# Kernel tuning notes

Measured on AMD Instinct MI355X. Metric: run time of the kernel, lower is better.

## Reference

```python
import jax, jax.numpy as jnp
import numpy as np

NUM_CLASSES = 80
STRIDES = (8, 16, 32)
FEAT_HW = ((80, 80), (40, 40), (20, 20))
B = 32
MAX_GT = 60


def setup_inputs() -> dict:
    key = jax.random.key(0)
    ks = jax.random.split(key, 6)
    feats = {}
    for i, (s, (h, w)) in enumerate(zip(STRIDES, FEAT_HW)):
        feats[f"feat{s}"] = jax.random.normal(ks[i], (B, 5 + NUM_CLASSES, h, w), jnp.float32)
    u = jax.random.uniform(ks[3], (B, MAX_GT, 4), jnp.float32)
    # cx,cy in [0,640), w,h in [8,128): realistic pixel-space gt boxes for a 640x640 image
    gt_boxes = jnp.concatenate([u[..., :2] * 640.0, u[..., 2:] * 120.0 + 8.0], -1)
    gt_classes = jax.random.randint(ks[4], (B, MAX_GT), 0, NUM_CLASSES)
    num_gts = jax.random.randint(ks[5], (B,), 1, MAX_GT + 1)
    return dict(feat8=feats["feat8"], feat16=feats["feat16"], feat32=feats["feat32"],
                gt_boxes=gt_boxes, gt_classes=gt_classes, num_gts=num_gts)


def _decode(feat, stride):
    # torch get_output_and_grid: xy=(raw+grid)*stride, wh=exp(raw)*stride
    b, c, h, w = feat.shape
    yv, xv = jnp.meshgrid(jnp.arange(h), jnp.arange(w), indexing="ij")
    gx = xv.reshape(-1).astype(feat.dtype)  # [H*W]
    gy = yv.reshape(-1).astype(feat.dtype)
    out = feat.reshape(b, c, h * w).transpose(0, 2, 1)  # [B,A,C]
    xy = (out[..., :2] + jnp.stack([gx, gy], -1)[None]) * stride
    wh = jnp.exp(out[..., 2:4]) * stride
    return jnp.concatenate([xy, wh, out[..., 4:]], -1), gx, gy


def _pair_iou(a, b):
    # a: [G,4] xywh, b: [A,4] xywh -> [G,A] IoU (bboxes_iou, xyxy=False)
    tl = jnp.maximum(a[:, None, :2] - a[:, None, 2:] * 0.5, b[None, :, :2] - b[None, :, 2:] * 0.5)
    br = jnp.minimum(a[:, None, :2] + a[:, None, 2:] * 0.5, b[None, :, :2] + b[None, :, 2:] * 0.5)
    en = jnp.all(tl < br, -1)
    inter = jnp.where(en, jnp.prod(br - tl, -1), 0.0)
    area_a = jnp.prod(a[:, 2:], -1)
    area_b = jnp.prod(b[:, 2:], -1)
    return inter / (area_a[:, None] + area_b[None, :] - inter + 1e-16)


def _bce_logits(x, t):
    return jnp.maximum(x, 0.0) - x * t + jnp.log1p(jnp.exp(-jnp.abs(x)))


def _iou_loss(pred, tgt):
    # IOUloss(loss_type='iou'): 1 - iou^2, per box
    tl = jnp.maximum(pred[..., :2] - pred[..., 2:] * 0.5, tgt[..., :2] - tgt[..., 2:] * 0.5)
    br = jnp.minimum(pred[..., :2] + pred[..., 2:] * 0.5, tgt[..., :2] + tgt[..., 2:] * 0.5)
    en = jnp.all(tl < br, -1)
    inter = jnp.where(en, jnp.prod(br - tl, -1), 0.0)
    union = jnp.prod(pred[..., 2:], -1) + jnp.prod(tgt[..., 2:], -1) - inter
    iou = inter / (union + 1e-16)
    return 1.0 - iou ** 2


def _assign(boxes, cls_lo, obj_lo, gtb, gtc, vmask, cx, cy, st):
    # SimOTA per image. boxes [A,4], cls_lo [A,C], obj_lo [A], gtb [G,4], gtc [G] int,
    # vmask [G] bool (gt padding), cx/cy/st [A] anchor centers & strides.
    G, A = gtb.shape[0], boxes.shape[0]
    iou = _pair_iou(gtb, boxes)  # [G,A]
    gx, gy = gtb[:, :1], gtb[:, 1:2]
    gw, gh = gtb[:, 2:3], gtb[:, 3:4]
    in_box = ((cx[None] > gx - 0.5 * gw) & (cx[None] < gx + 0.5 * gw) &
              (cy[None] > gy - 0.5 * gh) & (cy[None] < gy + 0.5 * gh))
    R = 2.5  # center sampling radius (in strides)
    in_ctr = ((cx[None] > gx - R * st[None]) & (cx[None] < gx + R * st[None]) &
              (cy[None] > gy - R * st[None]) & (cy[None] < gy + R * st[None]))
    fg = ((in_box | in_ctr) & vmask[:, None]).any(0)  # [A] candidate anchors
    in_both = (in_box & in_ctr).astype(boxes.dtype)
    # pairwise cls cost: BCE(sqrt(sig(cls)*sig(obj)), onehot(gt_cls)).sum(-1),
    # decomposed to avoid the [G,A,C] tensor: sum_c bce0 + (bce1-bce0)[gt_cls]
    p = jnp.clip(jnp.sqrt(jax.nn.sigmoid(cls_lo) * jax.nn.sigmoid(obj_lo)[:, None]), 1e-7, 1.0 - 1e-7)
    bce1 = -jnp.log(p)          # [A,C]
    bce0 = -jnp.log(1.0 - p)    # [A,C]
    cls_cost = bce0.sum(-1)[None, :] + (bce1 - bce0)[:, gtc].T  # [G,A]
    cost = (cls_cost + 3.0 * (-jnp.log(iou + 1e-8))
            + 100000.0 * (1.0 - in_both)
            + 1e9 * (~fg)[None, :].astype(boxes.dtype)
            + 1e9 * (~vmask)[:, None].astype(boxes.dtype))
    K = 10  # n_candidate_k
    topk_ious, _ = jax.lax.top_k(iou * fg[None, :], K)
    dyn_k = jnp.maximum(topk_ious.sum(-1).astype(jnp.int32), 1)  # clamp(int(sum), min=1)
    _, pos = jax.lax.top_k(-cost, K)  # [G,K] lowest-cost anchors per gt
    sel = (jnp.arange(K)[None, :] < dyn_k[:, None]).astype(boxes.dtype)
    matching = jnp.zeros((G, A), boxes.dtype).at[jnp.arange(G)[:, None], pos].set(sel)
    matching = matching * vmask[:, None].astype(boxes.dtype)
    # resolve anchors claimed by >1 gt: keep min-cost gt
    conflict = matching.sum(0) > 1
    best_gt = jnp.argmin(cost, axis=0)  # [A]
    matching = jnp.where(conflict[None, :], jax.nn.one_hot(best_gt, G, dtype=matching.dtype).T, matching)
    fg_final = matching.sum(0) > 0  # [A]
    matched = jnp.argmax(matching, axis=0)  # [A]
    pred_iou = (matching * iou).sum(0)  # [A]
    cls_t = jax.nn.one_hot(gtc[matched], NUM_CLASSES, dtype=boxes.dtype) * pred_iou[:, None]
    reg_t = gtb[matched]
    return fg_final, cls_t, reg_t


def _forward(feat8, feat16, feat32, gt_boxes, gt_classes, num_gts):
    outs, cxs, cys, sts = [], [], [], []
    for f, s in zip((feat8, feat16, feat32), STRIDES):
        o, gx, gy = _decode(f, float(s))
        outs.append(o)
        cxs.append((gx + 0.5) * s)
        cys.append((gy + 0.5) * s)
        sts.append(jnp.full_like(gx, s))
    preds = jnp.concatenate(outs, 1)  # [B,A,5+C]
    cx = jnp.concatenate(cxs)
    cy = jnp.concatenate(cys)
    st = jnp.concatenate(sts)
    boxes = preds[..., :4]
    obj_lo = preds[..., 4]
    cls_lo = preds[..., 5:]
    vmask = jnp.arange(MAX_GT)[None, :] < num_gts[:, None]
    fg, cls_t, reg_t = jax.vmap(_assign, in_axes=(0, 0, 0, 0, 0, 0, None, None, None))(
        boxes, cls_lo, obj_lo, gt_boxes, gt_classes, vmask, cx, cy, st)
    # SimOTA assignment is no_grad in YOLOX: targets are constants wrt preds
    fg = jax.lax.stop_gradient(fg)
    cls_t = jax.lax.stop_gradient(cls_t)
    reg_t = jax.lax.stop_gradient(reg_t)
    fg_f = fg.astype(boxes.dtype)
    num_fg = jnp.maximum(fg_f.sum(), 1.0)
    loss_iou = (_iou_loss(boxes, reg_t) * fg_f).sum()
    loss_obj = _bce_logits(obj_lo, fg_f * 0.9).sum()  # obj_targets * 0.9 smoothing
    loss_cls = (_bce_logits(cls_lo, cls_t) * fg_f[..., None]).sum()
    REG_WEIGHT = 5.0
    return (REG_WEIGHT * loss_iou + loss_obj + loss_cls) / num_fg


def reference(feat8, feat16, feat32, gt_boxes, gt_classes, num_gts):
    return _forward(feat8, feat16, feat32, gt_boxes, gt_classes, num_gts)
```

## Files before the change

kernel.cpp:

```cpp
#include <hip/hip_runtime.h>

constexpr int kB = 32;
constexpr int kA = 8400;
constexpr int kG = 60;
constexpr int kC = 80;
constexpr int kK = 10;
constexpr int kNBx = (kA + 255)/256;
constexpr int kNB = kNBx * kB;

__device__ __forceinline__ float fexp(float x){ return __expf(x); }
__device__ __forceinline__ float flog(float x){ return __logf(x); }
__device__ __forceinline__ float frcp(float x){ return __builtin_amdgcn_rcpf(x); }
__device__ __forceinline__ float frsq(float x){ return __builtin_amdgcn_rsqf(x); }
__device__ __forceinline__ float fsqrt(float x){ return __builtin_amdgcn_sqrtf(x); }
__device__ __forceinline__ float fdiv(float a, float b){ return a * __builtin_amdgcn_rcpf(b); }
__device__ __forceinline__ float sigm(float x){ return frcp(1.0f + fexp(-x)); }
__device__ __forceinline__ float bce(float x, float t){
  return fmaxf(x, 0.0f) - x*t + flog(1.0f + fexp(-fabsf(x)));
}

__device__ __forceinline__ unsigned ordbits(float v){
  unsigned u = __float_as_uint(v);
  return (u & 0x80000000u) ? ~u : (u | 0x80000000u);
}
__device__ __forceinline__ float unpackf(unsigned k){
  return __uint_as_float((k & 0x80000000u) ? (k & 0x7fffffffu) : ~k);
}

struct AInfo { int x, y; float st; };
__device__ __forceinline__ AInfo ainfo(int a){
  AInfo r;
  if (a < 6400)      { r.x = a % 80;           r.y = a / 80;           r.st = 8.0f;  }
  else if (a < 8000) { int l = a-6400; r.x = l % 40; r.y = l / 40;     r.st = 16.0f; }
  else               { int l = a-8000; r.x = l % 20; r.y = l / 20;     r.st = 32.0f; }
  return r;
}

__device__ __forceinline__ float featv(const float* __restrict__ f8,
                                       const float* __restrict__ f16,
                                       const float* __restrict__ f32x,
                                       int b, int ch, int a){
  if (a < 6400) return f8 [(b*85 + ch)*6400 + a];
  if (a < 8000) return f16[(b*85 + ch)*1600 + (a - 6400)];
  return             f32x[(b*85 + ch)*400  + (a - 8000)];
}

__device__ __forceinline__ float pair_iou(float4 g, float4 p){
  float tlx = fmaxf(g.x - g.z*0.5f, p.x - p.z*0.5f);
  float tly = fmaxf(g.y - g.w*0.5f, p.y - p.w*0.5f);
  float brx = fminf(g.x + g.z*0.5f, p.x + p.z*0.5f);
  float bry = fminf(g.y + g.w*0.5f, p.y + p.w*0.5f);
  float inter = (tlx < brx && tly < bry) ? (brx-tlx)*(bry-tly) : 0.0f;
  return fdiv(inter, g.z*g.w + p.z*p.w - inter + 1e-16f);
}

__device__ __forceinline__ float cost_core(float iou, float cl, float obs, float b0sum,
                                           int a, float4 gt, int fg_a){
  AInfo ai = ainfo(a);
  float cx = ((float)ai.x + 0.5f)*ai.st;
  float cy = ((float)ai.y + 0.5f)*ai.st;
  bool in_box = (cx > gt.x - 0.5f*gt.z) && (cx < gt.x + 0.5f*gt.z)
             && (cy > gt.y - 0.5f*gt.w) && (cy < gt.y + 0.5f*gt.w);
  bool in_ctr = (cx > gt.x - 2.5f*ai.st) && (cx < gt.x + 2.5f*ai.st)
             && (cy > gt.y - 2.5f*ai.st) && (cy < gt.y + 2.5f*ai.st);
  float p = fsqrt(sigm(cl) * obs);
  p = fminf(fmaxf(p, 1e-7f), 1.0f - 1e-7f);
  float diff = -flog(p) + flog(1.0f - p);
  float c = b0sum + diff;
  c += 3.0f * (-flog(iou + 1e-8f));
  c += (in_box && in_ctr) ? 0.0f : 100000.0f;
  c += fg_a ? 0.0f : 1000000000.0f;
  return c;
}

__device__ __forceinline__ unsigned long long wave_max64(unsigned long long v){
  #pragma unroll
  for (int off = 32; off; off >>= 1){
    unsigned long long o = __shfl_xor(v, off, 64);
    if (o > v) v = o;
  }
  return v;
}

__device__ __forceinline__ void stage16(const float* g, float* l){
  __builtin_amdgcn_global_load_lds(
      (const __attribute__((address_space(1))) void*)g,
      (__attribute__((address_space(3))) void*)l, 16, 0, 0);
}
__device__ __forceinline__ void wait_vm6(int n){
  if      (n >= 6) asm volatile("s_waitcnt vmcnt(6)" ::: "memory");
  else if (n >= 4) asm volatile("s_waitcnt vmcnt(4)" ::: "memory");
  else if (n >= 2) asm volatile("s_waitcnt vmcnt(2)" ::: "memory");
  else             asm volatile("s_waitcnt vmcnt(0)" ::: "memory");
  __builtin_amdgcn_sched_barrier(0);
}
__device__ __forceinline__ void block_bar(){
  __builtin_amdgcn_sched_barrier(0);
  __builtin_amdgcn_s_barrier();
  __builtin_amdgcn_sched_barrier(0);
}

__global__ __launch_bounds__(256) void k_decode(
    const float* __restrict__ f8, const float* __restrict__ f16, const float* __restrict__ f32x,
    const float* __restrict__ gtb, const int* __restrict__ ngts,
    float* __restrict__ boxes, float* __restrict__ boxesZ,
    float* __restrict__ objl, float* __restrict__ b0s,
    float* __restrict__ bceS, float* __restrict__ obsA,
    int* __restrict__ fg, int* __restrict__ cnt, int* __restrict__ mtch){
  int b = blockIdx.y;
  int tid = threadIdx.x;
  int lane = tid & 63, wid = tid >> 6;
  int a0 = blockIdx.x*256 + tid;
  bool alive = (a0 < kA);
  int a = alive ? a0 : (kA - 1);
  __shared__ float4 sg[kG];
  __shared__ float buf[8][4][256];
  if (tid < kG) sg[tid] = ((const float4*)gtb)[b*kG + tid];
  int ng = ngts[b];
  __syncthreads();

  const float* base; int hw, off; float st_; int gx, gy;
  if (a < 6400)      { base=f8;   hw=6400; off=a;        st_=8.0f;  gx=off%80; gy=off/80; }
  else if (a < 8000) { base=f16;  hw=1600; off=a-6400;   st_=16.0f; gx=off%40; gy=off/40; }
  else               { base=f32x; hw=400;  off=a-8000;   st_=32.0f; gx=off%20; gy=off/20; }
  const float* p0 = base + ((size_t)b*85)*hw + off;

  float t0 = p0[0];
  float t1 = p0[(size_t)hw];
  float t2 = p0[(size_t)2*hw];
  float t3 = p0[(size_t)3*hw];
  float ob = p0[(size_t)4*hw];
  __builtin_amdgcn_sched_barrier(0);

  bool pure = (blockIdx.x < 31);
  const float* csrc = nullptr;
  size_t lhw = 0;
  if (pure){
    int ab = blockIdx.x*256;
    const float* lv; int lh, lo_;
    if (ab < 6400){ lv = f8;  lh = 6400; lo_ = ab; }
    else          { lv = f16; lh = 1600; lo_ = ab - 6400; }
    lhw = (size_t)lh;
    csrc = lv + ((size_t)b*85 + 5)*lh + lo_ + lane*4;
    #pragma unroll
    for (int u = 0; u < 8; ++u)
      stage16(csrc + (size_t)(4*u + wid)*lhw, &buf[u][wid][0]);
  }
  __builtin_amdgcn_sched_barrier(0);

  float4 bx;
  bx.x = (t0 + (float)gx) * st_;
  bx.y = (t1 + (float)gy) * st_;
  bx.z = fexp(t2) * st_;
  bx.w = fexp(t3) * st_;
  float obs = sigm(ob);
  float so = fsqrt(obs);
  float cx = ((float)gx + 0.5f)*st_;
  float cy = ((float)gy + 0.5f)*st_;
  int f = 0;
  for (int g = 0; g < ng; ++g){
    float4 gt = sg[g];
    bool in_box = (cx > gt.x - 0.5f*gt.z) && (cx < gt.x + 0.5f*gt.z)
               && (cy > gt.y - 0.5f*gt.w) && (cy < gt.y + 0.5f*gt.w);
    bool in_ctr = (cx > gt.x - 2.5f*st_) && (cx < gt.x + 2.5f*st_)
               && (cy > gt.y - 2.5f*st_) && (cy < gt.y + 2.5f*st_);
    if (in_box || in_ctr){ f = 1; break; }
  }

  float s = 0.0f, sumCl = 0.0f, slogv = 0.0f;
  if (pure){
    #pragma unroll
    for (int g = 0; g < 10; ++g){
      const int allowed = (g < 6) ? 6 : (18 - 2*g);
      wait_vm6(allowed);
      block_bar();
      float cv[8];
      #pragma unroll
      for (int c = 0; c < 4; ++c) cv[c]     = buf[(2*g)   & 7][c][tid];
      #pragma unroll
      for (int c = 0; c < 4; ++c) cv[4 + c] = buf[(2*g+1) & 7][c][tid];
      asm volatile("s_waitcnt lgkmcnt(0)" ::: "memory");
      __builtin_amdgcn_sched_barrier(0);
      block_bar();
      if (g < 6){
        stage16(csrc + (size_t)(4*(2*g+8) + wid)*lhw, &buf[(2*g)   & 7][wid][0]);
        stage16(csrc + (size_t)(4*(2*g+9) + wid)*lhw, &buf[(2*g+1) & 7][wid][0]);
      }
      __builtin_amdgcn_sched_barrier(0);
      float prodS = 1.0f, prodV = 1.0f;
      #pragma unroll
      for (int j = 0; j < 8; ++j){
        float c = cv[j];
        float u = fexp(-c);
        float v = 1.0f + u;
        float p = so * frsq(v);
        p = fminf(fmaxf(p, 1e-7f), 1.0f - 1e-7f);
        prodS *= (1.0f - p);
        prodV *= v;
        sumCl += c;
      }
      s -= flog(prodS);
      slogv += flog(prodV);
    }
  } else {
    const float* pc = p0 + (size_t)5*hw;
    #pragma unroll 1
    for (int grp = 0; grp < kC/8; ++grp){
      float prodS = 1.0f, prodV = 1.0f;
      #pragma unroll
      for (int j = 0; j < 8; ++j){
        float c = pc[(size_t)(grp*8 + j)*hw];
        float u = fexp(-c);
        float v = 1.0f + u;
        float p = so * frsq(v);
        p = fminf(fmaxf(p, 1e-7f), 1.0f - 1e-7f);
        prodS *= (1.0f - p);
        prodV *= v;
        sumCl += c;
      }
      s -= flog(prodS);
      slogv += flog(prodV);
    }
  }
  __builtin_amdgcn_sched_barrier(0);
  if (alive){
    int idx = b*kA + a;
    ((float4*)boxes)[idx] = bx;
    objl[idx] = ob;
    obsA[idx] = obs;
    cnt[idx] = 0;
    mtch[idx] = 0x7fffffff;
    fg[idx] = f;
    ((float4*)boxesZ)[idx] = f ? bx : make_float4(0.0f,0.0f,0.0f,0.0f);
    b0s[idx]  = s;
    bceS[idx] = sumCl + slogv;
  }
}

__global__ __launch_bounds__(256) void k_assign(
    const float* __restrict__ f8, const float* __restrict__ f16, const float* __restrict__ f32x,
    const float* __restrict__ gtb, const int* __restrict__ gtc, const int* __restrict__ ngts,
    const float* __restrict__ boxes, const float* __restrict__ boxesZ,
    const float* __restrict__ obsA, const float* __restrict__ b0s,
    const int* __restrict__ fg,
    int* __restrict__ cnt, int* __restrict__ mtch){
  int b = blockIdx.x / kG;
  int g = blockIdx.x % kG;
  if (g >= ngts[b]) return;
  int tid = threadIdx.x;
  int lane = tid & 63, wid = tid >> 6;
  float4 gt = ((const float4*)gtb)[b*kG + g];
  int cls = gtc[b*kG + g];
  const float4* bx4 = (const float4*)boxes;
  const float4* bzp = (const float4*)boxesZ + (size_t)b*kA;
  const float* c8  = f8   + ((size_t)b*85 + 5 + cls)*6400;
  const float* c16 = f16  + ((size_t)b*85 + 5 + cls)*1600;
  const float* c32 = f32x + ((size_t)b*85 + 5 + cls)*400;

  __shared__ unsigned long long lds_k[4*kK];
  __shared__ int lds_cnt[4];
  __shared__ int s_dynk;

  unsigned long long k1[kK];
  #pragma unroll
  for (int i = 0; i < kK; ++i) k1[i] = 0ull;

  auto ins = [&](unsigned long long key){
    if (key > k1[kK-1]){
      k1[kK-1] = key;
      #pragma unroll
      for (int q = kK-1; q > 0; --q)
        if (k1[q] > k1[q-1]){ unsigned long long t = k1[q]; k1[q] = k1[q-1]; k1[q-1] = t; }
    }
  };

  for (int i0 = tid; i0 < kA; i0 += 2048){
    float4 cbox[8];
    unsigned long long kk[8];
    #pragma unroll
    for (int u = 0; u < 8; ++u){
      int iu = i0 + u*256;
      cbox[u] = bzp[(iu < kA) ? iu : (kA-1)];
    }
    unsigned long long mx = 0ull;
    #pragma unroll
    for (int u = 0; u < 8; ++u){
      int iu = i0 + u*256;
      float v = pair_iou(gt, cbox[u]);
      kk[u] = (iu < kA) ? (((unsigned long long)ordbits(v) << 32) | (unsigned)(~iu)) : 0ull;
      if (kk[u] > mx) mx = kk[u];
    }
    if (mx > k1[kK-1]){
      #pragma unroll
      for (int u = 0; u < 8; ++u) ins(kk[u]);
    }
  }
  {
    unsigned long long wtop = 0ull;
    #pragma unroll
    for (int k = 0; k < kK; ++k){
      unsigned long long best = wave_max64(k1[0]);
      if (k1[0] == best){
        #pragma unroll
        for (int i2_ = 0; i2_ < kK-1; ++i2_) k1[i2_] = k1[i2_+1];
        k1[kK-1] = 0ull;
      }
      if (lane == k) wtop = best;
    }
    if (lane < kK) lds_k[wid*kK + lane] = wtop;
  }
  __syncthreads();
  if (wid == 0){
    unsigned long long key = (lane < 4*kK) ? lds_k[lane] : 0ull;
    float ksum = 0.0f;
    #pragma unroll
    for (int k = 0; k < kK; ++k){
      unsigned long long best = wave_max64(key);
      if (key == best) key = 0ull;
      if (best) ksum += unpackf((unsigned)(best >> 32));
    }
    if (lane == 0) s_dynk = max((int)ksum, 1);
  }
  __syncthreads();
  int dynk = s_dynk;

  int x00,y00,nx0,n0, x01,y01,nx1,n1, x02,y02,nx2,n2;
  {
    auto rect = [&](float st, int W, int& rx0, int& ry0, int& rnx, int& rn){
      float lox = fmaxf(gt.x - 0.5f*gt.z, gt.x - 2.5f*st);
      float hix = fminf(gt.x + 0.5f*gt.z, gt.x + 2.5f*st);
      float loy = fmaxf(gt.y - 0.5f*gt.w, gt.y - 2.5f*st);
      float hiy = fminf(gt.y + 0.5f*gt.w, gt.y + 2.5f*st);
      float rs = frcp(st);
      int ax0 = max(0,   (int)floorf(lox*rs - 0.5f) - 1);
      int ax1 = min(W-1, (int)ceilf (hix*rs - 0.5f) + 1);
      int ay0 = max(0,   (int)floorf(loy*rs - 0.5f) - 1);
      int ay1 = min(W-1, (int)ceilf (hiy*rs - 0.5f) + 1);
      rx0 = ax0; ry0 = ay0;
      rnx = max(0, ax1 - ax0 + 1);
      int rny = max(0, ay1 - ay0 + 1);
      rn = rnx * rny;
    };
    rect( 8.0f, 80, x00, y00, nx0, n0);
    rect(16.0f, 40, x01, y01, nx1, n1);
    rect(32.0f, 20, x02, y02, nx2, n2);
  }
  int total = n0 + n1 + n2;

  unsigned long long ck = 0ull;
  int nvalid = 0;
  if (tid < total){
    int i = tid, ix, iy, a; float st;
    if (i < n0)           { ix = x00 + i % nx0; iy = y00 + i / nx0; a = iy*80 + ix;          st = 8.0f;  }
    else if (i < n0 + n1) { int j = i - n0;      ix = x01 + j % nx1; iy = y01 + j / nx1; a = 6400 + iy*40 + ix; st = 16.0f; }
    else                  { int j = i - n0 - n1; ix = x02 + j % nx2; iy = y02 + j / nx2; a = 8000 + iy*20 + ix; st = 32.0f; }
    float cx = ((float)ix + 0.5f)*st;
    float cy = ((float)iy + 0.5f)*st;
    bool in_box = (cx > gt.x - 0.5f*gt.z) && (cx < gt.x + 0.5f*gt.z)
               && (cy > gt.y - 0.5f*gt.w) && (cy < gt.y + 0.5f*gt.w);
    bool in_ctr = (cx > gt.x - 2.5f*st) && (cx < gt.x + 2.5f*st)
               && (cy > gt.y - 2.5f*st) && (cy < gt.y + 2.5f*st);
    if (in_box && in_ctr){
      int idx = b*kA + a;
      float4 bx = bx4[idx];
      float iou = pair_iou(gt, bx);
      float cl = (a < 6400) ? c8[a] : (a < 8000) ? c16[a-6400] : c32[a-8000];
      float c = cost_core(iou, cl, obsA[idx], b0s[idx], a, gt, 1);
      ck = ~(((unsigned long long)ordbits(c) << 32) | (unsigned)a);
      nvalid = 1;
    }
  }
  {
    unsigned long long bal = __ballot(nvalid);
    if (lane == 0) lds_cnt[wid] = __popcll(bal);
    unsigned long long wtop = 0ull;
    #pragma unroll
    for (int k = 0; k < kK; ++k){
      unsigned long long best = wave_max64(ck);
      if (ck == best) ck = 0ull;
      if (lane == k) wtop = best;
    }
    if (lane < kK) lds_k[wid*kK + lane] = wtop;
  }
  __syncthreads();
  int cnt_total = lds_cnt[0] + lds_cnt[1] + lds_cnt[2] + lds_cnt[3];
  bool fb = (dynk > cnt_total);

  if (!fb){
    if (wid == 0){
      unsigned long long key = (lane < 4*kK) ? lds_k[lane] : 0ull;
      unsigned long long mine = 0ull;
      #pragma unroll
      for (int k = 0; k < kK; ++k){
        unsigned long long best = wave_max64(key);
        if (key == best) key = 0ull;
        if (lane == k) mine = best;
      }
      if (lane < dynk && mine){
        int a = (int)((unsigned)(~mine));
        atomicAdd(&cnt[b*kA + a], 1);
        atomicMin(&mtch[b*kA + a], g);
      }
    }
    return;
  }

  __syncthreads();
  unsigned long long k2[kK];
  #pragma unroll
  for (int i = 0; i < kK; ++i) k2[i] = 0ull;
  for (int i = tid; i < kA; i += 256){
    int idx = b*kA + i;
    float4 bx = bx4[idx];
    float iou = pair_iou(gt, bx);
    int fga = fg[idx];
    float cl = (i < 6400) ? c8[i] : (i < 8000) ? c16[i-6400] : c32[i-8000];
    float c = cost_core(iou, cl, obsA[idx], b0s[idx], i, gt, fga);
    unsigned long long key2 = ~(((unsigned long long)ordbits(c) << 32) | (unsigned)i);
    if (key2 > k2[kK-1]){
      k2[kK-1] = key2;
      #pragma unroll
      for (int i2_ = kK-1; i2_ > 0; --i2_)
        if (k2[i2_] > k2[i2_-1]){ unsigned long long t = k2[i2_]; k2[i2_] = k2[i2_-1]; k2[i2_-1] = t; }
    }
  }
  {
    unsigned long long wtop = 0ull;
    #pragma unroll
    for (int k = 0; k < kK; ++k){
      unsigned long long best = wave_max64(k2[0]);
      if (k2[0] == best){
        #pragma unroll
        for (int i2_ = 0; i2_ < kK-1; ++i2_) k2[i2_] = k2[i2_+1];
        k2[kK-1] = 0ull;
      }
      if (lane == k) wtop = best;
    }
    if (lane < kK) lds_k[wid*kK + lane] = wtop;
  }
  __syncthreads();
  if (wid == 0){
    unsigned long long key = (lane < 4*kK) ? lds_k[lane] : 0ull;
    unsigned long long mine = 0ull;
    #pragma unroll
    for (int k = 0; k < kK; ++k){
      unsigned long long best = wave_max64(key);
      if (key == best) key = 0ull;
      if (lane == k) mine = best;
    }
    if (lane < dynk && mine){
      int a = (int)((unsigned)(~mine));
      atomicAdd(&cnt[b*kA + a], 1);
      atomicMin(&mtch[b*kA + a], g);
    }
  }
}

__global__ __launch_bounds__(256) void k_loss(
    const float* __restrict__ f8, const float* __restrict__ f16, const float* __restrict__ f32x,
    const float* __restrict__ gtb, const int* __restrict__ gtc, const int* __restrict__ ngts,
    const float* __restrict__ boxes, const float* __restrict__ objl, const float* __restrict__ b0s,
    const float* __restrict__ bceS, const float* __restrict__ obsA,
    const int* __restrict__ fg, const int* __restrict__ cnt, const int* __restrict__ mtch,
    float4* __restrict__ pacc){
  int b = blockIdx.y;
  int a = blockIdx.x*256 + threadIdx.x;
  int tid = threadIdx.x;
  __shared__ float4 sg[kG];
  __shared__ int scls[kG];
  if (tid < kG){ sg[tid] = ((const float4*)gtb)[b*kG + tid]; scls[tid] = gtc[b*kG + tid]; }
  bool valid = (a < kA);
  int idx = valid ? (b*kA + a) : (b*kA);
  int c      = valid ? cnt[idx]  : 0;
  float ob   = valid ? objl[idx] : 0.0f;
  float4 bx  = valid ? ((const float4*)boxes)[idx] : make_float4(0,0,1,1);
  int mg_raw = valid ? mtch[idx] : 0;
  float b0   = valid ? b0s[idx]  : 0.0f;
  float obs  = valid ? obsA[idx] : 0.0f;
  int fga    = valid ? fg[idx]   : 0;
  float bS   = valid ? bceS[idx] : 0.0f;
  __syncthreads();
  float li = 0.0f, lo = 0.0f, lc = 0.0f, nf = 0.0f;

  float fgf = 0.0f; int mg = 0;
  if (valid && c == 1){ mg = mg_raw; fgf = 1.0f; }
  bool need = valid && (c > 1);
  if (__any(need)){
    if (need){
      int ng = ngts[b];
      float bestc = 3.0e38f; int bg = 0;
      for (int g = 0; g < ng; ++g){
        float iou = pair_iou(sg[g], bx);
        float cl = featv(f8,f16,f32x,b,5+scls[g],a);
        float cst = cost_core(iou, cl, obs, b0, a, sg[g], fga);
        if (cst < bestc){ bestc = cst; bg = g; }
      }
      mg = bg; fgf = 1.0f;
    }
  }
  if (valid){
    lo = bce(ob, fgf*0.9f);
    if (fgf > 0.0f){
      nf = 1.0f;
      float4 r = sg[mg];
      float piou = pair_iou(r, bx);
      float tlx = fmaxf(bx.x - bx.z*0.5f, r.x - r.z*0.5f);
      float tly = fmaxf(bx.y - bx.w*0.5f, r.y - r.w*0.5f);
      float brx = fminf(bx.x + bx.z*0.5f, r.x + r.z*0.5f);
      float bry = fminf(bx.y + bx.w*0.5f, r.y + r.w*0.5f);
      float inter = (tlx < brx && tly < bry) ? (brx-tlx)*(bry-tly) : 0.0f;
      float un = bx.z*bx.w + r.z*r.w - inter;
      float iou = fdiv(inter, un + 1e-16f);
      li = 1.0f - iou*iou;
      int tc = scls[mg];
      float cl_tc = featv(f8,f16,f32x,b,5+tc,a);
      lc = bS - piou * cl_tc;
    }
  }
  for (int off = 32; off > 0; off >>= 1){
    li += __shfl_down(li, off, 64);
    lo += __shfl_down(lo, off, 64);
    lc += __shfl_down(lc, off, 64);
    nf += __shfl_down(nf, off, 64);
  }
  __shared__ float4 wred[4];
  int wid = tid >> 6;
  if ((tid & 63) == 0) wred[wid] = make_float4(li, lo, lc, nf);
  __syncthreads();
  if (tid == 0){
    float4 t = wred[0];
    for (int w = 1; w < 4; ++w){
      float4 o = wred[w];
      t.x += o.x; t.y += o.y; t.z += o.z; t.w += o.w;
    }
    pacc[blockIdx.y * gridDim.x + blockIdx.x] = t;
  }
}

__global__ __launch_bounds__(256) void k_final(
    const float4* __restrict__ pacc, float* __restrict__ out){
  int tid = threadIdx.x;
  float li = 0.0f, lo = 0.0f, lc = 0.0f, nf = 0.0f;
  for (int i = tid; i < kNB; i += 256){
    float4 p = pacc[i];
    li += p.x; lo += p.y; lc += p.z; nf += p.w;
  }
  for (int off = 32; off > 0; off >>= 1){
    li += __shfl_down(li, off, 64);
    lo += __shfl_down(lo, off, 64);
    lc += __shfl_down(lc, off, 64);
    nf += __shfl_down(nf, off, 64);
  }
  __shared__ float4 wred[4];
  int wid = tid >> 6;
  if ((tid & 63) == 0) wred[wid] = make_float4(li, lo, lc, nf);
  __syncthreads();
  if (tid == 0){
    float4 t = wred[0];
    for (int w = 1; w < 4; ++w){
      float4 o = wred[w];
      t.x += o.x; t.y += o.y; t.z += o.z; t.w += o.w;
    }
    out[0] = (5.0f*t.x + t.y + t.z) * frcp(fmaxf(t.w, 1.0f));
  }
}

extern "C" void kernel_launch(void* const* d_in, const int* in_sizes, int n_in,
                              void* d_out, int out_size, void* d_ws, size_t ws_size,
                              hipStream_t stream) {
  (void)in_sizes; (void)n_in; (void)out_size; (void)ws_size;
  const float* f8   = (const float*)d_in[0];
  const float* f16  = (const float*)d_in[1];
  const float* f32x = (const float*)d_in[2];
  const float* gtb  = (const float*)d_in[3];
  const int*   gtc  = (const int*)d_in[4];
  const int*   ngts = (const int*)d_in[5];
  float* out = (float*)d_out;

  const size_t BA = (size_t)kB*kA;
  float* ws     = (float*)d_ws;
  float* boxes  = ws;
  float* boxesZ = boxes  + BA*4;
  float* objl   = boxesZ + BA*4;
  float* b0s    = objl   + BA;
  float* bceS   = b0s    + BA;
  float* obsA   = bceS   + BA;
  int*   fg     = (int*)(obsA + BA);
  int*   cnt    = fg  + BA;
  int*   mtch   = cnt + BA;
  float4* pacc  = (float4*)(mtch + BA);

  dim3 gBA(kNBx, kB);
  k_decode<<<gBA, dim3(256), 0, stream>>>(f8,f16,f32x,gtb,ngts,boxes,boxesZ,objl,b0s,bceS,obsA,fg,cnt,mtch);
  k_assign<<<dim3(kB*kG), dim3(256), 0, stream>>>(f8,f16,f32x,gtb,gtc,ngts,boxes,boxesZ,obsA,b0s,fg,cnt,mtch);
  k_loss<<<gBA, dim3(256), 0, stream>>>(f8,f16,f32x,gtb,gtc,ngts,boxes,objl,b0s,bceS,obsA,fg,cnt,mtch,pacc);
  k_final<<<dim3(1), dim3(256), 0, stream>>>(pacc, out);
}
```

Before: 201.3 us.

## Split decode class-reduction across two blocks per anchor chunk with atomic accumulation

The decode kernel now launches two blocks per 256-anchor chunk, each reducing half of the 80 class channels, and combines the partial b0s/bceS sums with atomicAdd after a memset zeroes them. The LDS staging switches from 16-byte per-lane global_load_lds to 4-byte per-lane loads with a per-wave double buffer and no block barriers, and it applies uniformly including the tail block. The goal is more blocks in flight and less barrier stalling in a memory-bound kernel. The cost is an extra memset launch, float atomics, narrower load transactions, and a nondeterministic summation order.

```diff
diff --git a/kernel.cpp b/kernel.cpp
--- a/kernel.cpp
+++ b/kernel.cpp
@@ -82,21 +82,14 @@
   return v;
 }
 
-__device__ __forceinline__ void stage16(const float* g, float* l){
+__device__ __forceinline__ void stage1(const float* g, float* l){
   __builtin_amdgcn_global_load_lds(
       (const __attribute__((address_space(1))) void*)g,
-      (__attribute__((address_space(3))) void*)l, 16, 0, 0);
-}
-__device__ __forceinline__ void wait_vm6(int n){
-  if      (n >= 6) asm volatile("s_waitcnt vmcnt(6)" ::: "memory");
-  else if (n >= 4) asm volatile("s_waitcnt vmcnt(4)" ::: "memory");
-  else if (n >= 2) asm volatile("s_waitcnt vmcnt(2)" ::: "memory");
-  else             asm volatile("s_waitcnt vmcnt(0)" ::: "memory");
-  __builtin_amdgcn_sched_barrier(0);
-}
-__device__ __forceinline__ void block_bar(){
-  __builtin_amdgcn_sched_barrier(0);
-  __builtin_amdgcn_s_barrier();
+      (__attribute__((address_space(3))) void*)l, 4, 0, 0);
+}
+__device__ __forceinline__ void wait_vm8(int n){
+  if (n >= 8) asm volatile("s_waitcnt vmcnt(8)" ::: "memory");
+  else        asm volatile("s_waitcnt vmcnt(0)" ::: "memory");
   __builtin_amdgcn_sched_barrier(0);
 }
 
@@ -107,15 +100,17 @@
     float* __restrict__ objl, float* __restrict__ b0s,
     float* __restrict__ bceS, float* __restrict__ obsA,
     int* __restrict__ fg, int* __restrict__ cnt, int* __restrict__ mtch){
+  int chunk = blockIdx.x >> 1;
+  int j     = blockIdx.x & 1;
   int b = blockIdx.y;
   int tid = threadIdx.x;
-  int lane = tid & 63, wid = tid >> 6;
-  int a0 = blockIdx.x*256 + tid;
+  int wid = tid >> 6;
+  int a0 = chunk*256 + tid;
   bool alive = (a0 < kA);
   int a = alive ? a0 : (kA - 1);
   __shared__ float4 sg[kG];
-  __shared__ float buf[8][4][256];
-  if (tid < kG) sg[tid] = ((const float4*)gtb)[b*kG + tid];
+  __shared__ float buf[2][8][256];
+  if (j == 0 && tid < kG) sg[tid] = ((const float4*)gtb)[b*kG + tid];
   int ng = ngts[b];
   __syncthreads();
 
@@ -124,116 +119,91 @@
   else if (a < 8000) { base=f16;  hw=1600; off=a-6400;   st_=16.0f; gx=off%40; gy=off/40; }
   else               { base=f32x; hw=400;  off=a-8000;   st_=32.0f; gx=off%20; gy=off/20; }
   const float* p0 = base + ((size_t)b*85)*hw + off;
-
-  float t0 = p0[0];
-  float t1 = p0[(size_t)hw];
-  float t2 = p0[(size_t)2*hw];
-  float t3 = p0[(size_t)3*hw];
+  const float* pc = p0 + (size_t)5*hw;
+  int wbase = wid * 64;
+  int gbase = j * 5;
+
   float ob = p0[(size_t)4*hw];
+  float t0 = 0.0f, t1 = 0.0f, t2 = 0.0f, t3 = 0.0f;
+  if (j == 0){
+    t0 = p0[0];
+    t1 = p0[(size_t)hw];
+    t2 = p0[(size_t)2*hw];
+    t3 = p0[(size_t)3*hw];
+  }
   __builtin_amdgcn_sched_barrier(0);
-
-  bool pure = (blockIdx.x < 31);
-  const float* csrc = nullptr;
-  size_t lhw = 0;
-  if (pure){
-    int ab = blockIdx.x*256;
-    const float* lv; int lh, lo_;
-    if (ab < 6400){ lv = f8;  lh = 6400; lo_ = ab; }
-    else          { lv = f16; lh = 1600; lo_ = ab - 6400; }
-    lhw = (size_t)lh;
-    csrc = lv + ((size_t)b*85 + 5)*lh + lo_ + lane*4;
-    #pragma unroll
-    for (int u = 0; u < 8; ++u)
-      stage16(csrc + (size_t)(4*u + wid)*lhw, &buf[u][wid][0]);
-  }
+  #pragma unroll
+  for (int u = 0; u < 2; ++u)
+    #pragma unroll
+    for (int jj = 0; jj < 8; ++jj)
+      stage1(pc + (size_t)((gbase + u)*8 + jj)*hw, &buf[u][jj][wbase]);
   __builtin_amdgcn_sched_barrier(0);
 
-  float4 bx;
-  bx.x = (t0 + (float)gx) * st_;
-  bx.y = (t1 + (float)gy) * st_;
-  bx.z = fexp(t2) * st_;
-  bx.w = fexp(t3) * st_;
   float obs = sigm(ob);
   float so = fsqrt(obs);
-  float cx = ((float)gx + 0.5f)*st_;
-  float cy = ((float)gy + 0.5f)*st_;
+  float4 bx = make_float4(0,0,0,0);
   int f = 0;
-  for (int g = 0; g < ng; ++g){
-    float4 gt = sg[g];
-    bool in_box = (cx > gt.x - 0.5f*gt.z) && (cx < gt.x + 0.5f*gt.z)
-               && (cy > gt.y - 0.5f*gt.w) && (cy < gt.y + 0.5f*gt.w);
-    bool in_ctr = (cx > gt.x - 2.5f*st_) && (cx < gt.x + 2.5f*st_)
-               && (cy > gt.y - 2.5f*st_) && (cy < gt.y + 2.5f*st_);
-    if (in_box || in_ctr){ f = 1; break; }
+  if (j == 0){
+    bx.x = (t0 + (float)gx) * st_;
+    bx.y = (t1 + (float)gy) * st_;
+    bx.z = fexp(t2) * st_;
+    bx.w = fexp(t3) * st_;
+    float cx = ((float)gx + 0.5f)*st_;
+    float cy = ((float)gy + 0.5f)*st_;
+    for (int g = 0; g < ng; ++g){
+      float4 gt = sg[g];
+      bool in_box = (cx > gt.x - 0.5f*gt.z) && (cx < gt.x + 0.5f*gt.z)
+                 && (cy > gt.y - 0.5f*gt.w) && (cy < gt.y + 0.5f*gt.w);
+      bool in_ctr = (cx > gt.x - 2.5f*st_) && (cx < gt.x + 2.5f*st_)
+                 && (cy > gt.y - 2.5f*st_) && (cy < gt.y + 2.5f*st_);
+      if (in_box || in_ctr){ f = 1; break; }
+    }
   }
 
   float s = 0.0f, sumCl = 0.0f, slogv = 0.0f;
-  if (pure){
-    #pragma unroll
-    for (int g = 0; g < 10; ++g){
-      const int allowed = (g < 6) ? 6 : (18 - 2*g);
-      wait_vm6(allowed);
-      block_bar();
-      float cv[8];
+  #pragma unroll
+  for (int g = 0; g < 5; ++g){
+    wait_vm8((g < 4) ? 8 : 0);
+    float cv[8];
+    #pragma unroll
+    for (int jj = 0; jj < 8; ++jj) cv[jj] = buf[g & 1][jj][tid];
+    asm volatile("s_waitcnt lgkmcnt(0)" ::: "memory");
+    __builtin_amdgcn_sched_barrier(0);
+    if (g + 2 < 5){
       #pragma unroll
-      for (int c = 0; c < 4; ++c) cv[c]     = buf[(2*g)   & 7][c][tid];
-      #pragma unroll
-      for (int c = 0; c < 4; ++c) cv[4 + c] = buf[(2*g+1) & 7][c][tid];
-      asm volatile("s_waitcnt lgkmcnt(0)" ::: "memory");
-      __builtin_amdgcn_sched_barrier(0);
-      block_bar();
-      if (g < 6){
-        stage16(csrc + (size_t)(4*(2*g+8) + wid)*lhw, &buf[(2*g)   & 7][wid][0]);
-        stage16(csrc + (size_t)(4*(2*g+9) + wid)*lhw, &buf[(2*g+1) & 7][wid][0]);
-      }
-      __builtin_amdgcn_sched_barrier(0);
-      float prodS = 1.0f, prodV = 1.0f;
-      #pragma unroll
-      for (int j = 0; j < 8; ++j){
-        float c = cv[j];
-        float u = fexp(-c);
-        float v = 1.0f + u;
-        float p = so * frsq(v);
-        p = fminf(fmaxf(p, 1e-7f), 1.0f - 1e-7f);
-        prodS *= (1.0f - p);
-        prodV *= v;
-        sumCl += c;
-      }
-      s -= flog(prodS);
-      slogv += flog(prodV);
-    }
-  } else {
-    const float* pc = p0 + (size_t)5*hw;
-    #pragma unroll 1
-    for (int grp = 0; grp < kC/8; ++grp){
-      float prodS = 1.0f, prodV = 1.0f;
-      #pragma unroll
-      for (int j = 0; j < 8; ++j){
-        float c = pc[(size_t)(grp*8 + j)*hw];
-        float u = fexp(-c);
-        float v = 1.0f + u;
-        float p = so * frsq(v);
-        p = fminf(fmaxf(p, 1e-7f), 1.0f - 1e-7f);
-        prodS *= (1.0f - p);
-        prodV *= v;
-        sumCl += c;
-      }
-      s -= flog(prodS);
-      slogv += flog(prodV);
-    }
+      for (int jj = 0; jj < 8; ++jj)
+        stage1(pc + (size_t)((gbase + g + 2)*8 + jj)*hw, &buf[g & 1][jj][wbase]);
+    }
+    __builtin_amdgcn_sched_barrier(0);
+    float prodS = 1.0f, prodV = 1.0f;
+    #pragma unroll
+    for (int jj = 0; jj < 8; ++jj){
+      float c = cv[jj];
+      float u = fexp(-c);
+      float v = 1.0f + u;
+      float p = so * frsq(v);
+      p = fminf(fmaxf(p, 1e-7f), 1.0f - 1e-7f);
+      prodS *= (1.0f - p);
+      prodV *= v;
+      sumCl += c;
+    }
+    s -= flog(prodS);
+    slogv += flog(prodV);
   }
   __builtin_amdgcn_sched_barrier(0);
   if (alive){
     int idx = b*kA + a;
-    ((float4*)boxes)[idx] = bx;
-    objl[idx] = ob;
-    obsA[idx] = obs;
-    cnt[idx] = 0;
-    mtch[idx] = 0x7fffffff;
-    fg[idx] = f;
-    ((float4*)boxesZ)[idx] = f ? bx : make_float4(0.0f,0.0f,0.0f,0.0f);
-    b0s[idx]  = s;
-    bceS[idx] = sumCl + slogv;
+    if (j == 0){
+      ((float4*)boxes)[idx] = bx;
+      objl[idx] = ob;
+      obsA[idx] = obs;
+      cnt[idx] = 0;
+      mtch[idx] = 0x7fffffff;
+      fg[idx] = f;
+      ((float4*)boxesZ)[idx] = f ? bx : make_float4(0.0f,0.0f,0.0f,0.0f);
+    }
+    atomicAdd(&b0s[idx],  s);
+    atomicAdd(&bceS[idx], sumCl + slogv);
   }
 }
 
@@ -352,8 +322,8 @@
   if (tid < total){
     int i = tid, ix, iy, a; float st;
     if (i < n0)           { ix = x00 + i % nx0; iy = y00 + i / nx0; a = iy*80 + ix;          st = 8.0f;  }
-    else if (i < n0 + n1) { int j = i - n0;      ix = x01 + j % nx1; iy = y01 + j / nx1; a = 6400 + iy*40 + ix; st = 16.0f; }
-    else                  { int j = i - n0 - n1; ix = x02 + j % nx2; iy = y02 + j / nx2; a = 8000 + iy*20 + ix; st = 32.0f; }
+    else if (i < n0 + n1) { int jj = i - n0;      ix = x01 + jj % nx1; iy = y01 + jj / nx1; a = 6400 + iy*40 + ix; st = 16.0f; }
+    else                  { int jj = i - n0 - n1; ix = x02 + jj % nx2; iy = y02 + jj / nx2; a = 8000 + iy*20 + ix; st = 32.0f; }
     float cx = ((float)ix + 0.5f)*st;
     float cy = ((float)iy + 0.5f)*st;
     bool in_box = (cx > gt.x - 0.5f*gt.z) && (cx < gt.x + 0.5f*gt.z)
@@ -590,9 +560,11 @@
   int*   mtch   = cnt + BA;
   float4* pacc  = (float4*)(mtch + BA);
 
+  hipMemsetAsync(b0s, 0, 2*BA*sizeof(float), stream);
+  dim3 gD(2*kNBx, kB);
+  k_decode<<<gD, dim3(256), 0, stream>>>(f8,f16,f32x,gtb,ngts,boxes,boxesZ,objl,b0s,bceS,obsA,fg,cnt,mtch);
+  k_assign<<<dim3(kB*kG), dim3(256), 0, stream>>>(f8,f16,f32x,gtb,gtc,ngts,boxes,boxesZ,obsA,b0s,fg,cnt,mtch);
   dim3 gBA(kNBx, kB);
-  k_decode<<<gBA, dim3(256), 0, stream>>>(f8,f16,f32x,gtb,ngts,boxes,boxesZ,objl,b0s,bceS,obsA,fg,cnt,mtch);
-  k_assign<<<dim3(kB*kG), dim3(256), 0, stream>>>(f8,f16,f32x,gtb,gtc,ngts,boxes,boxesZ,obsA,b0s,fg,cnt,mtch);
   k_loss<<<gBA, dim3(256), 0, stream>>>(f8,f16,f32x,gtb,gtc,ngts,boxes,objl,b0s,bceS,obsA,fg,cnt,mtch,pacc);
   k_final<<<dim3(1), dim3(256), 0, stream>>>(pacc, out);
 }
```

Measured after the change: 210.2 us. 1.04x slower.
